# Kernel tuning notes

Measured on AMD Instinct MI355X. Metric: run time of the kernel, lower is better.

Reference implementation:

```python
import jax, jax.numpy as jnp
import numpy as np

NPOINT, RADIUS, NSAMPLE = 512, 0.2, 32
EPS = 1e-5
CHANNELS = [67, 64, 64, 128]


def _fps(pts, npoint):
    # pts: [B, N, 3]; deterministic start at index 0 (torch impl uses randint)
    B, N, _ = pts.shape
    def body(carry, _):
        mind, far = carry
        c = jnp.take_along_axis(pts, far[:, None, None], axis=1)         # [B,1,3]
        mind = jnp.minimum(mind, jnp.sum((pts - c) ** 2, axis=-1))
        return (mind, jnp.argmax(mind, axis=-1).astype(jnp.int32)), far
    init = (jnp.full((B, N), 1e10, pts.dtype), jnp.zeros((B,), jnp.int32))
    _, idxs = jax.lax.scan(body, init, None, length=npoint)
    return idxs.T                                                         # [B, npoint]


def _gather(p, idx):
    # p: [B, N, C], idx: [B, ...] -> [B, ..., C]
    return jax.vmap(lambda pp, ii: pp[ii])(p, idx)


def _cbr(x, w, b, g, be, m, v):
    # Conv3d kernel [1, 4, 1]; torch padding='same' on even kernel -> (lo=1, hi=2) on t axis
    y = jax.lax.conv_general_dilated(x, w, (1, 1, 1),
                                     [(0, 0), (1, 2), (0, 0)],
                                     dimension_numbers=('NCDHW', 'OIDHW', 'NCDHW'))
    ex = lambda a: a[None, :, None, None, None]
    y = y + ex(b)
    # BatchNorm3d (eval mode with running stats)
    y = (y - ex(m)) * ex(g / jnp.sqrt(v + EPS)) + ex(be)
    return jax.nn.relu(y)


def _forward(xyz, points, params):
    B, t, _, N = xyz.shape
    S, K = NPOINT, NSAMPLE
    xf = jnp.transpose(xyz, (0, 1, 3, 2)).reshape(B * t, N, 3)            # [BT,N,3]
    pf = jnp.transpose(points, (0, 1, 3, 2)).reshape(B * t, N, -1)        # [BT,N,D]
    fidx = _fps(xf.reshape(B, t, N, 3)[:, 0], S)                          # [B,S], FPS on frame 0
    fidx_bt = jnp.broadcast_to(fidx[:, None, :], (B, t, S)).reshape(B * t, S)
    new_xyz = _gather(xf, fidx_bt)                                        # [BT,S,3]
    # squared distances via matmul form (matches square_distance)
    sq = (jnp.sum(new_xyz ** 2, -1)[:, :, None] + jnp.sum(xf ** 2, -1)[:, None, :]
          - 2.0 * jnp.einsum('bsc,bnc->bsn', new_xyz, xf))                # [BT,S,N]
    # ball query: invalid -> N, sort indices, take first K, fallback to first valid
    gidx = jnp.where(sq > RADIUS ** 2, N, jnp.arange(N, dtype=jnp.int32)[None, None, :])
    gidx = jnp.sort(gidx, axis=-1)[:, :, :K]                              # [BT,S,K]
    gidx = jnp.where(gidx == N, gidx[:, :, :1], gidx)
    gxyz = _gather(xf, gidx) - new_xyz[:, :, None, :]                     # [BT,S,K,3]
    feat = jnp.concatenate([gxyz, _gather(pf, gidx)], axis=-1)            # [BT,S,K,3+D]
    feat = feat.reshape(B, t, S, K, -1).transpose(0, 4, 2, 1, 3)          # [B,C,S,t,K]
    for p in params:
        feat = _cbr(feat, *p)
    feat = jnp.max(feat, axis=-1)                                         # [B,C',S,t]
    new_points = jnp.transpose(feat, (0, 3, 1, 2))                        # [B,t,C',S]
    new_xyz = new_xyz.reshape(B, t, S, 3).transpose(0, 1, 3, 2)           # [B,t,3,S]
    return new_xyz, new_points


def setup_inputs() -> dict:
    key = jax.random.key(0)
    ks = jax.random.split(key, 40)
    B, t, D, N = 2, 8, 64, 1024
    inp = {
        'xyz': jax.random.uniform(ks[0], (B, t, 3, N), jnp.float32),
        'points': jax.random.normal(ks[1], (B, t, D, N), jnp.float32),
    }
    j = 2
    for i in range(3):
        ci, co = CHANNELS[i], CHANNELS[i + 1]
        inp[f'w{i}'] = jax.random.normal(ks[j], (co, ci, 1, 4, 1), jnp.float32) * 0.05; j += 1
        inp[f'b{i}'] = jax.random.normal(ks[j], (co,), jnp.float32) * 0.01; j += 1
        inp[f'g{i}'] = jax.random.uniform(ks[j], (co,), jnp.float32, 0.5, 1.5); j += 1
        inp[f'be{i}'] = jax.random.normal(ks[j], (co,), jnp.float32) * 0.1; j += 1
        inp[f'm{i}'] = jax.random.normal(ks[j], (co,), jnp.float32) * 0.1; j += 1
        inp[f'v{i}'] = jax.random.uniform(ks[j], (co,), jnp.float32, 0.5, 1.5); j += 1
    return inp


def reference(xyz, points, w0, b0, g0, be0, m0, v0, w1, b1, g1, be1, m1, v1, w2, b2, g2, be2, m2, v2):
    params = [(w0, b0, g0, be0, m0, v0), (w1, b1, g1, be1, m1, v1), (w2, b2, g2, be2, m2, v2)]
    return _forward(xyz, points, params)
```

## Files before the change

### kernel.cpp

```cpp
#include <hip/hip_runtime.h>
#include <math.h>

#define NPTS 1024
#define S_   512
#define T_   8
#define K_   32
#define B_   2

typedef short bf16x8 __attribute__((ext_vector_type(8)));
typedef short short4v __attribute__((ext_vector_type(4)));
typedef float f32x4 __attribute__((ext_vector_type(4)));
typedef float vf2 __attribute__((ext_vector_type(2)));

static __device__ __forceinline__ short f2bf(float f) {
    unsigned u = __float_as_uint(f);
    unsigned r = (u + 0x7FFFu + ((u >> 16) & 1u)) >> 16;
    return (short)r;
}

template <int CTRL>
static __device__ __forceinline__ float dppmaxf(float x) {
    int mv = __builtin_amdgcn_update_dpp(0, __float_as_int(x), CTRL, 0xF, 0xF, true);
    return fmaxf(x, __int_as_float(mv));
}
static __device__ __forceinline__ unsigned wavemax_bits_f(float x) {
    x = dppmaxf<0x111>(x); x = dppmaxf<0x112>(x);
    x = dppmaxf<0x114>(x); x = dppmaxf<0x118>(x);
    x = dppmaxf<0x142>(x); x = dppmaxf<0x143>(x);
    return (unsigned)__builtin_amdgcn_readlane(__float_as_int(x), 63);
}

static __device__ __forceinline__ vf2 pk_sub(vf2 a, vf2 b) { return a - b; }
static __device__ __forceinline__ vf2 pk_fma(vf2 a, vf2 b, vf2 c) {
#if __has_builtin(__builtin_elementwise_fma)
    return __builtin_elementwise_fma(a, b, c);
#else
    vf2 r; r[0] = __fmaf_rn(a[0], b[0], c[0]); r[1] = __fmaf_rn(a[1], b[1], c[1]); return r;
#endif
}
static __device__ __forceinline__ vf2 pk_min(vf2 a, vf2 b) {
#if __has_builtin(__builtin_elementwise_min)
    return __builtin_elementwise_min(a, b);
#else
    vf2 r; r[0] = fminf(a[0], b[0]); r[1] = fminf(a[1], b[1]); return r;
#endif
}
static __device__ __forceinline__ vf2 pk_max(vf2 a, vf2 b) {
#if __has_builtin(__builtin_elementwise_max)
    return __builtin_elementwise_max(a, b);
#else
    vf2 r; r[0] = fmaxf(a[0], b[0]); r[1] = fmaxf(a[1], b[1]); return r;
#endif
}

__global__ __launch_bounds__(64) void fps_kernel(const float* __restrict__ xyz,
                                                 int* __restrict__ fidx)
{
    int b    = blockIdx.x;
    int lane = threadIdx.x;
    __shared__ float4 sc[NPTS];
    const float* bx = xyz + (size_t)b * (T_ * 3 * NPTS);
    vf2 px2[8], py2[8], pz2[8], mind2[8];
#pragma unroll
    for (int q = 0; q < 4; ++q) {
        float4 vx = ((const float4*)(bx))[lane * 4 + q];
        float4 vy = ((const float4*)(bx + NPTS))[lane * 4 + q];
        float4 vz = ((const float4*)(bx + 2 * NPTS))[lane * 4 + q];
        px2[q*2]   = (vf2){vx.x, vx.y};  px2[q*2+1] = (vf2){vx.z, vx.w};
        py2[q*2]   = (vf2){vy.x, vy.y};  py2[q*2+1] = (vf2){vy.z, vy.w};
        pz2[q*2]   = (vf2){vz.x, vz.y};  pz2[q*2+1] = (vf2){vz.z, vz.w};
        int n0 = lane * 16 + q * 4;
        sc[n0+0] = make_float4(vx.x, vy.x, vz.x, 0.f);
        sc[n0+1] = make_float4(vx.y, vy.y, vz.y, 0.f);
        sc[n0+2] = make_float4(vx.z, vy.z, vz.z, 0.f);
        sc[n0+3] = make_float4(vx.w, vy.w, vz.w, 0.f);
        mind2[q*2] = (vf2){1e10f, 1e10f}; mind2[q*2+1] = (vf2){1e10f, 1e10f};
    }
    __syncthreads();

    int far = 0;
    for (int it = 0; it < S_; ++it) {
        if (lane == 0) fidx[b * S_ + it] = far;
        float4 c = sc[far];
        vf2 c2x = (vf2){c.x, c.x}, c2y = (vf2){c.y, c.y}, c2z = (vf2){c.z, c.z};
#pragma unroll
        for (int q = 0; q < 8; ++q) {
            vf2 dx = pk_sub(px2[q], c2x);
            vf2 dy = pk_sub(py2[q], c2y);
            vf2 dz = pk_sub(pz2[q], c2z);
            vf2 d  = pk_fma(dz, dz, pk_fma(dy, dy, dx * dx));
            mind2[q] = pk_min(mind2[q], d);
        }
        vf2 t4a = pk_max(mind2[0], mind2[4]);
        vf2 t4b = pk_max(mind2[1], mind2[5]);
        vf2 t4c = pk_max(mind2[2], mind2[6]);
        vf2 t4d = pk_max(mind2[3], mind2[7]);
        vf2 t2a = pk_max(t4a, t4c);
        vf2 t2b = pk_max(t4b, t4d);
        vf2 t1  = pk_max(t2a, t2b);
        float lmax = fmaxf(t1[0], t1[1]);
        unsigned maxb = wavemax_bits_f(lmax);
        int cj[16];
#pragma unroll
        for (int j = 0; j < 16; ++j)
            cj[j] = (__float_as_uint(mind2[j >> 1][j & 1]) == maxb) ? j : 64;
        int m8[8], m4[4], m2v[2];
#pragma unroll
        for (int j = 0; j < 8; ++j) m8[j] = min(cj[j], cj[j + 8]);
#pragma unroll
        for (int j = 0; j < 4; ++j) m4[j] = min(m8[j], m8[j + 4]);
        m2v[0] = min(m4[0], m4[2]); m2v[1] = min(m4[1], m4[3]);
        int minj = min(m2v[0], m2v[1]);
        unsigned long long mk = __ballot(minj < 64);
        int l0 = __ffsll((long long)mk) - 1;
        int jw = __builtin_amdgcn_readlane(minj, l0);
        far = l0 * 16 + jw;
    }
}

__global__ __launch_bounds__(256) void transpose_points(
    const float* __restrict__ pts, short* __restrict__ ptsT)
{
    int nt = blockIdx.x;
    int bt = blockIdx.y;
    __shared__ float tile[64][65];
    int tid = threadIdx.x;
    for (int e = tid; e < 4096; e += 256) {
        int ci = e >> 6, nn = e & 63;
        tile[ci][nn] = pts[((size_t)bt * 64 + ci) * NPTS + nt * 64 + nn];
    }
    __syncthreads();
    for (int e = tid; e < 4096; e += 256) {
        int nn = e >> 6, ci = e & 63;
        ptsT[((size_t)bt * NPTS + nt * 64 + nn) * 64 + ci] = f2bf(tile[ci][nn]);
    }
}

template <int CI, int CIp, int CO, bool PERM>
__global__ __launch_bounds__(256) void prep_w(const float* __restrict__ w,
                                              short* __restrict__ wg)
{
    int e = blockIdx.x * 256 + threadIdx.x;
    if (e >= 4 * CO * CIp) return;
    int dt = e / (CO * CIp);
    int rem = e - dt * (CO * CIp);
    int co = rem / CIp;
    int ci = rem - co * CIp;
    float val = 0.0f;
    if (PERM) {
        int cref = (ci < 64) ? (ci + 3) : ((ci < 67) ? (ci - 64) : -1);
        if (cref >= 0) val = w[((size_t)co * CI + cref) * 4 + dt];
    } else {
        if (ci < CI) val = w[((size_t)co * CI + ci) * 4 + dt];
    }
    wg[e] = f2bf(val);
}

__global__ __launch_bounds__(256) void conv1_fused(
    const float* __restrict__ xyz, const short* __restrict__ ptsT,
    const int* __restrict__ fidx,
    const short* __restrict__ wg, const float* __restrict__ bb,
    const float* __restrict__ gg, const float* __restrict__ be,
    const float* __restrict__ mm, const float* __restrict__ vv,
    short* __restrict__ actOut, float* __restrict__ out0)
{
    const int CIp = 104, NK = 3, CO = 64;
    __shared__ __align__(16) short xs[256 * 104];
    __shared__ int   gidx_l[8][K_];
    __shared__ float nxyz_l[8][3];
    int s = blockIdx.x, b = blockIdx.y;
    int tid = threadIdx.x;
    int lane = tid & 63;
    int wv   = tid >> 6;

    int fid = fidx[b * S_ + s];
    for (int half = 0; half < 2; ++half) {
        int tt = wv * 2 + half;
        int bt = b * T_ + tt;
        const float* bx = xyz + (size_t)bt * 3 * NPTS;
        float nx = bx[fid], ny = bx[NPTS + fid], nz = bx[2 * NPTS + fid];
        if (lane < 3) {
            float vvv = (lane == 0) ? nx : ((lane == 1) ? ny : nz);
            out0[(bt * 3 + lane) * S_ + s] = vvv;
            nxyz_l[tt][lane] = vvv;
        }
        float A = __fmaf_rn(nz, nz, __fmaf_rn(ny, ny, __fmul_rn(nx, nx)));
        const float R2 = (float)(0.2 * 0.2);
        int count = 0, firstIdx = -1;
        for (int j = 0; j < 16; ++j) {
            if (count >= K_) break;
            int n = j * 64 + lane;
            float x = bx[n], y = bx[NPTS + n], z = bx[2 * NPTS + n];
            float Bn = __fmaf_rn(z, z, __fmaf_rn(y, y, __fmul_rn(x, x)));
            float C  = __fmaf_rn(nz, z, __fmaf_rn(ny, y, __fmul_rn(nx, x)));
            float sq = __fsub_rn(__fadd_rn(A, Bn), __fmul_rn(2.0f, C));
            bool valid = !(sq > R2);
            unsigned long long mb = __ballot(valid);
            if (valid) {
                int pos = count + __popcll(mb & ((1ull << lane) - 1ull));
                if (pos < K_) gidx_l[tt][pos] = n;
            }
            if (firstIdx < 0 && mb) firstIdx = j * 64 + (__ffsll((long long)mb) - 1);
            count += __popcll(mb);
        }
        if (count < K_) {
            for (int p = count + lane; p < K_; p += 64) gidx_l[tt][p] = firstIdx;
        }
    }
    __syncthreads();

    {
        int col = tid;
        int k = col & 31, tt = col >> 5;
        int bt = b * T_ + tt;
        short* xrow = &xs[col * CIp];
        int idx = gidx_l[tt][k];
        const short* prow = ptsT + ((size_t)bt * NPTS + idx) * 64;
#pragma unroll
        for (int c = 0; c < 8; ++c)
            ((int4*)xrow)[c] = ((const int4*)prow)[c];
#pragma unroll
        for (int ci = 0; ci < 3; ++ci)
            xrow[64 + ci] = f2bf(xyz[(size_t)(bt * 3 + ci) * NPTS + idx] - nxyz_l[tt][ci]);
        for (int ci = 67; ci < CIp; ++ci) xrow[ci] = 0;
    }
    __syncthreads();

    int l16 = lane & 15, lq = lane >> 4;
    f32x4 acc[16];
#pragma unroll
    for (int nb = 0; nb < 16; ++nb) acc[nb] = (f32x4){0.f, 0.f, 0.f, 0.f};
#pragma unroll
    for (int ks = 0; ks < NK; ++ks) {
        bf16x8 afr[4];
#pragma unroll
        for (int dt = 0; dt < 4; ++dt)
            afr[dt] = *(const bf16x8*)&wg[((size_t)(dt * CO + wv * 16 + l16)) * CIp + ks * 32 + lq * 8];
        bf16x8 bfr[16];
#pragma unroll
        for (int cb = 0; cb < 16; ++cb)
            bfr[cb] = *(const bf16x8*)&xs[(cb * 16 + l16) * CIp + ks * 32 + lq * 8];
#pragma unroll
        for (int dt = 0; dt < 4; ++dt) {
#pragma unroll
            for (int nb = 0; nb < 16; ++nb) {
                int cb = nb + (dt - 1) * 2;
                if (cb >= 0 && cb < 16)
                    acc[nb] = __builtin_amdgcn_mfma_f32_16x16x32_bf16(
                        afr[dt], bfr[cb], acc[nb], 0, 0, 0);
            }
        }
    }
    float sc[4], c2[4];
#pragma unroll
    for (int j = 0; j < 4; ++j) {
        int co = wv * 16 + lq * 4 + j;
        float scv = gg[co] / sqrtf(vv[co] + 1e-5f);
        sc[j] = scv;
        c2[j] = (bb[co] - mm[co]) * scv + be[co];
    }
#pragma unroll
    for (int nb = 0; nb < 16; ++nb) {
        int col = nb * 16 + l16;
        short4v pk;
#pragma unroll
        for (int j = 0; j < 4; ++j)
            pk[j] = f2bf(fmaxf(acc[nb][j] * sc[j] + c2[j], 0.0f));
        *(short4v*)&actOut[(((size_t)b * S_ + s) * 256 + col) * 64 + wv * 16 + lq * 4] = pk;
    }
}

__global__ __launch_bounds__(256) void conv23_fused(
    const short* __restrict__ actIn,
    const short* __restrict__ wg1, const float* __restrict__ bb1,
    const float* __restrict__ gg1, const float* __restrict__ be1,
    const float* __restrict__ mm1, const float* __restrict__ vv1,
    const short* __restrict__ wg2, const float* __restrict__ bb2,
    const float* __restrict__ gg2, const float* __restrict__ be2,
    const float* __restrict__ mm2, const float* __restrict__ vv2,
    float* __restrict__ outPool)
{
    const int CIp = 72, NK = 2;
    __shared__ __align__(16) short xs2[256 * 72];
    __shared__ __align__(16) short xs3[256 * 72];
    int s = blockIdx.x, b = blockIdx.y;
    int tid = threadIdx.x;
    int lane = tid & 63;
    int wv   = tid >> 6;
    int l16  = lane & 15;
    int lq   = lane >> 4;

    {
        int col = tid;
        short* xrow = &xs2[col * CIp];
        const short* src = actIn + (((size_t)b * S_ + s) * 256 + col) * 64;
#pragma unroll
        for (int c = 0; c < 8; ++c)
            ((int4*)xrow)[c] = ((const int4*)src)[c];
        short* xrow3 = &xs3[col * CIp];
        for (int ci = 64; ci < CIp; ++ci) { xrow[ci] = 0; xrow3[ci] = 0; }
    }
    __syncthreads();

    {
        f32x4 acc[16];
#pragma unroll
        for (int nb = 0; nb < 16; ++nb) acc[nb] = (f32x4){0.f, 0.f, 0.f, 0.f};
#pragma unroll
        for (int ks = 0; ks < NK; ++ks) {
            bf16x8 afr[4];
#pragma unroll
            for (int dt = 0; dt < 4; ++dt)
                afr[dt] = *(const bf16x8*)&wg1[((size_t)(dt * 64 + wv * 16 + l16)) * CIp + ks * 32 + lq * 8];
            bf16x8 bfr[16];
#pragma unroll
            for (int cb = 0; cb < 16; ++cb)
                bfr[cb] = *(const bf16x8*)&xs2[(cb * 16 + l16) * CIp + ks * 32 + lq * 8];
#pragma unroll
            for (int dt = 0; dt < 4; ++dt) {
#pragma unroll
                for (int nb = 0; nb < 16; ++nb) {
                    int cb = nb + (dt - 1) * 2;
                    if (cb >= 0 && cb < 16)
                        acc[nb] = __builtin_amdgcn_mfma_f32_16x16x32_bf16(
                            afr[dt], bfr[cb], acc[nb], 0, 0, 0);
                }
            }
        }
        float sc[4], c2[4];
#pragma unroll
        for (int j = 0; j < 4; ++j) {
            int co = wv * 16 + lq * 4 + j;
            float scv = gg1[co] / sqrtf(vv1[co] + 1e-5f);
            sc[j] = scv;
            c2[j] = (bb1[co] - mm1[co]) * scv + be1[co];
        }
#pragma unroll
        for (int nb = 0; nb < 16; ++nb) {
            int col = nb * 16 + l16;
            short4v pk;
#pragma unroll
            for (int j = 0; j < 4; ++j)
                pk[j] = f2bf(fmaxf(acc[nb][j] * sc[j] + c2[j], 0.0f));
            *(short4v*)&xs3[col * CIp + wv * 16 + lq * 4] = pk;
        }
    }
    __syncthreads();

#pragma unroll
    for (int st = 0; st < 2; ++st) {
        f32x4 acc[16];
#pragma unroll
        for (int nb = 0; nb < 16; ++nb) acc[nb] = (f32x4){0.f, 0.f, 0.f, 0.f};
#pragma unroll
        for (int ks = 0; ks < NK; ++ks) {
            bf16x8 afr[4];
#pragma unroll
            for (int dt = 0; dt < 4; ++dt)
                afr[dt] = *(const bf16x8*)&wg2[((size_t)(dt * 128 + st * 64 + wv * 16 + l16)) * CIp + ks * 32 + lq * 8];
            bf16x8 bfr[16];
#pragma unroll
            for (int cb = 0; cb < 16; ++cb)
                bfr[cb] = *(const bf16x8*)&xs3[(cb * 16 + l16) * CIp + ks * 32 + lq * 8];
#pragma unroll
            for (int dt = 0; dt < 4; ++dt) {
#pragma unroll
                for (int nb = 0; nb < 16; ++nb) {
                    int cb = nb + (dt - 1) * 2;
                    if (cb >= 0 && cb < 16)
                        acc[nb] = __builtin_amdgcn_mfma_f32_16x16x32_bf16(
                            afr[dt], bfr[cb], acc[nb], 0, 0, 0);
                }
            }
        }
        float sc[4], c2[4];
#pragma unroll
        for (int j = 0; j < 4; ++j) {
            int co = st * 64 + wv * 16 + lq * 4 + j;
            float scv = gg2[co] / sqrtf(vv2[co] + 1e-5f);
            sc[j] = scv;
            c2[j] = (bb2[co] - mm2[co]) * scv + be2[co];
        }
#pragma unroll
        for (int nbp = 0; nbp < 8; ++nbp) {
#pragma unroll
            for (int j = 0; j < 4; ++j) {
                float v0 = fmaxf(acc[2 * nbp][j] * sc[j] + c2[j], 0.0f);
                float v1 = fmaxf(acc[2 * nbp + 1][j] * sc[j] + c2[j], 0.0f);
                float v = fmaxf(v0, v1);
#pragma unroll
                for (int off = 1; off < 16; off <<= 1)
                    v = fmaxf(v, __shfl_xor(v, off));
                if (l16 == 0) {
                    int co = st * 64 + wv * 16 + lq * 4 + j;
                    outPool[((size_t)(b * T_ + nbp) * 128 + co) * S_ + s] = v;
                }
            }
        }
    }
}

extern "C" void kernel_launch(void* const* d_in, const int* in_sizes, int n_in,
                              void* d_out, int out_size, void* d_ws, size_t ws_size,
                              hipStream_t stream)
{
    (void)in_sizes; (void)n_in; (void)out_size; (void)ws_size;
    const float* xyz    = (const float*)d_in[0];
    const float* points = (const float*)d_in[1];
    const float* w0 = (const float*)d_in[2];
    const float* b0 = (const float*)d_in[3];
    const float* g0 = (const float*)d_in[4];
    const float* be0 = (const float*)d_in[5];
    const float* m0 = (const float*)d_in[6];
    const float* v0 = (const float*)d_in[7];
    const float* w1 = (const float*)d_in[8];
    const float* b1 = (const float*)d_in[9];
    const float* g1 = (const float*)d_in[10];
    const float* be1 = (const float*)d_in[11];
    const float* m1 = (const float*)d_in[12];
    const float* v1 = (const float*)d_in[13];
    const float* w2 = (const float*)d_in[14];
    const float* b2 = (const float*)d_in[15];
    const float* g2 = (const float*)d_in[16];
    const float* be2 = (const float*)d_in[17];
    const float* m2 = (const float*)d_in[18];
    const float* v2 = (const float*)d_in[19];

    float* out = (float*)d_out;
    char* ws = (char*)d_ws;
    int*   fidx = (int*)ws;
    short* wg0  = (short*)(ws + (size_t)(3 * 1024 * 1024));
    short* wg1  = (short*)(ws + (size_t)(3 * 1024 * 1024) + 256 * 1024);
    short* wg2  = (short*)(ws + (size_t)(3 * 1024 * 1024) + 512 * 1024);
    short* ptsT = (short*)(ws + (size_t)(4  * 1024 * 1024));
    short* actA = (short*)(ws + (size_t)(8  * 1024 * 1024));

    prep_w<67, 104, 64,  true ><<<(4 * 64  * 104 + 255) / 256, 256, 0, stream>>>(w0, wg0);
    prep_w<64, 72,  64,  false><<<(4 * 64  * 72  + 255) / 256, 256, 0, stream>>>(w1, wg1);
    prep_w<64, 72,  128, false><<<(4 * 128 * 72  + 255) / 256, 256, 0, stream>>>(w2, wg2);
    transpose_points<<<dim3(16, B_ * T_), 256, 0, stream>>>(points, ptsT);
    fps_kernel<<<B_, 64, 0, stream>>>(xyz, fidx);

    conv1_fused<<<dim3(S_, B_), 256, 0, stream>>>(
        xyz, ptsT, fidx, wg0, b0, g0, be0, m0, v0, actA, out);
    conv23_fused<<<dim3(S_, B_), 256, 0, stream>>>(
        actA, wg1, b1, g1, be1, m1, v1, wg2, b2, g2, be2, m2, v2,
        out + (size_t)B_ * T_ * 3 * S_);
}
```

Measured before the change: 354.3 us.

## Fuse all three conv stages into one kernel and merge weight prep launches

Measured after the change: 355.0 us. No clear change (+0.2%).

```diff
diff --git a/kernel.cpp b/kernel.cpp
--- a/kernel.cpp
+++ b/kernel.cpp
@@ -136,42 +136,70 @@
     }
 }
 
-template <int CI, int CIp, int CO, bool PERM>
-__global__ __launch_bounds__(256) void prep_w(const float* __restrict__ w,
-                                              short* __restrict__ wg)
+__global__ __launch_bounds__(256) void prep_all(
+    const float* __restrict__ w0, const float* __restrict__ w1,
+    const float* __restrict__ w2,
+    short* __restrict__ wg0, short* __restrict__ wg1, short* __restrict__ wg2)
 {
+    int z = blockIdx.y;
     int e = blockIdx.x * 256 + threadIdx.x;
-    if (e >= 4 * CO * CIp) return;
-    int dt = e / (CO * CIp);
-    int rem = e - dt * (CO * CIp);
-    int co = rem / CIp;
-    int ci = rem - co * CIp;
-    float val = 0.0f;
-    if (PERM) {
+    if (z == 0) {
+        const int CI = 67, CIp = 100, CO = 64;
+        if (e >= 4 * CO * CIp) return;
+        int dt = e / (CO * CIp);
+        int rem = e - dt * (CO * CIp);
+        int co = rem / CIp;
+        int ci = rem - co * CIp;
+        float val = 0.0f;
         int cref = (ci < 64) ? (ci + 3) : ((ci < 67) ? (ci - 64) : -1);
-        if (cref >= 0) val = w[((size_t)co * CI + cref) * 4 + dt];
+        if (cref >= 0) val = w0[((size_t)co * CI + cref) * 4 + dt];
+        wg0[e] = f2bf(val);
+    } else if (z == 1) {
+        const int CI = 64, CIp = 72, CO = 64;
+        if (e >= 4 * CO * CIp) return;
+        int dt = e / (CO * CIp);
+        int rem = e - dt * (CO * CIp);
+        int co = rem / CIp;
+        int ci = rem - co * CIp;
+        wg1[e] = f2bf((ci < CI) ? w1[((size_t)co * CI + ci) * 4 + dt] : 0.0f);
     } else {
-        if (ci < CI) val = w[((size_t)co * CI + ci) * 4 + dt];
-    }
-    wg[e] = f2bf(val);
-}
-
-__global__ __launch_bounds__(256) void conv1_fused(
+        const int CI = 64, CIp = 72, CO = 128;
+        if (e >= 4 * CO * CIp) return;
+        int dt = e / (CO * CIp);
+        int rem = e - dt * (CO * CIp);
+        int co = rem / CIp;
+        int ci = rem - co * CIp;
+        wg2[e] = f2bf((ci < CI) ? w2[((size_t)co * CI + ci) * 4 + dt] : 0.0f);
+    }
+}
+
+__global__ __launch_bounds__(256) void conv123(
     const float* __restrict__ xyz, const short* __restrict__ ptsT,
     const int* __restrict__ fidx,
-    const short* __restrict__ wg, const float* __restrict__ bb,
-    const float* __restrict__ gg, const float* __restrict__ be,
-    const float* __restrict__ mm, const float* __restrict__ vv,
-    short* __restrict__ actOut, float* __restrict__ out0)
+    const short* __restrict__ wg0, const float* __restrict__ bb0,
+    const float* __restrict__ gg0, const float* __restrict__ be0,
+    const float* __restrict__ mm0, const float* __restrict__ vv0,
+    const short* __restrict__ wg1, const float* __restrict__ bb1,
+    const float* __restrict__ gg1, const float* __restrict__ be1,
+    const float* __restrict__ mm1, const float* __restrict__ vv1,
+    const short* __restrict__ wg2, const float* __restrict__ bb2,
+    const float* __restrict__ gg2, const float* __restrict__ be2,
+    const float* __restrict__ mm2, const float* __restrict__ vv2,
+    float* __restrict__ out0, float* __restrict__ outPool)
 {
-    const int CIp = 104, NK = 3, CO = 64;
-    __shared__ __align__(16) short xs[256 * 104];
+    const int CIp1 = 100, NK1 = 3;
+    const int CIp2 = 72,  NK2 = 2;
+    __shared__ __align__(16) short xsA[256 * CIp1];
     __shared__ int   gidx_l[8][K_];
     __shared__ float nxyz_l[8][3];
+    short* xsB = xsA;
+
     int s = blockIdx.x, b = blockIdx.y;
     int tid = threadIdx.x;
     int lane = tid & 63;
     int wv   = tid >> 6;
+    int l16  = lane & 15;
+    int lq   = lane >> 4;
 
     int fid = fidx[b * S_ + s];
     for (int half = 0; half < 2; ++half) {
@@ -187,8 +215,8 @@
         float A = __fmaf_rn(nz, nz, __fmaf_rn(ny, ny, __fmul_rn(nx, nx)));
         const float R2 = (float)(0.2 * 0.2);
         int count = 0, firstIdx = -1;
+#pragma unroll
         for (int j = 0; j < 16; ++j) {
-            if (count >= K_) break;
             int n = j * 64 + lane;
             float x = bx[n], y = bx[NPTS + n], z = bx[2 * NPTS + n];
             float Bn = __fmaf_rn(z, z, __fmaf_rn(y, y, __fmul_rn(x, x)));
@@ -213,7 +241,7 @@
         int col = tid;
         int k = col & 31, tt = col >> 5;
         int bt = b * T_ + tt;
-        short* xrow = &xs[col * CIp];
+        short* xrow = &xsA[col * CIp1];
         int idx = gidx_l[tt][k];
         const short* prow = ptsT + ((size_t)bt * NPTS + idx) * 64;
 #pragma unroll
@@ -222,83 +250,7 @@
 #pragma unroll
         for (int ci = 0; ci < 3; ++ci)
             xrow[64 + ci] = f2bf(xyz[(size_t)(bt * 3 + ci) * NPTS + idx] - nxyz_l[tt][ci]);
-        for (int ci = 67; ci < CIp; ++ci) xrow[ci] = 0;
-    }
-    __syncthreads();
-
-    int l16 = lane & 15, lq = lane >> 4;
-    f32x4 acc[16];
-#pragma unroll
-    for (int nb = 0; nb < 16; ++nb) acc[nb] = (f32x4){0.f, 0.f, 0.f, 0.f};
-#pragma unroll
-    for (int ks = 0; ks < NK; ++ks) {
-        bf16x8 afr[4];
-#pragma unroll
-        for (int dt = 0; dt < 4; ++dt)
-            afr[dt] = *(const bf16x8*)&wg[((size_t)(dt * CO + wv * 16 + l16)) * CIp + ks * 32 + lq * 8];
-        bf16x8 bfr[16];
-#pragma unroll
-        for (int cb = 0; cb < 16; ++cb)
-            bfr[cb] = *(const bf16x8*)&xs[(cb * 16 + l16) * CIp + ks * 32 + lq * 8];
-#pragma unroll
-        for (int dt = 0; dt < 4; ++dt) {
-#pragma unroll
-            for (int nb = 0; nb < 16; ++nb) {
-                int cb = nb + (dt - 1) * 2;
-                if (cb >= 0 && cb < 16)
-                    acc[nb] = __builtin_amdgcn_mfma_f32_16x16x32_bf16(
-                        afr[dt], bfr[cb], acc[nb], 0, 0, 0);
-            }
-        }
-    }
-    float sc[4], c2[4];
-#pragma unroll
-    for (int j = 0; j < 4; ++j) {
-        int co = wv * 16 + lq * 4 + j;
-        float scv = gg[co] / sqrtf(vv[co] + 1e-5f);
-        sc[j] = scv;
-        c2[j] = (bb[co] - mm[co]) * scv + be[co];
-    }
-#pragma unroll
-    for (int nb = 0; nb < 16; ++nb) {
-        int col = nb * 16 + l16;
-        short4v pk;
-#pragma unroll
-        for (int j = 0; j < 4; ++j)
-            pk[j] = f2bf(fmaxf(acc[nb][j] * sc[j] + c2[j], 0.0f));
-        *(short4v*)&actOut[(((size_t)b * S_ + s) * 256 + col) * 64 + wv * 16 + lq * 4] = pk;
-    }
-}
-
-__global__ __launch_bounds__(256) void conv23_fused(
-    const short* __restrict__ actIn,
-    const short* __restrict__ wg1, const float* __restrict__ bb1,
-    const float* __restrict__ gg1, const float* __restrict__ be1,
-    const float* __restrict__ mm1, const float* __restrict__ vv1,
-    const short* __restrict__ wg2, const float* __restrict__ bb2,
-    const float* __restrict__ gg2, const float* __restrict__ be2,
-    const float* __restrict__ mm2, const float* __restrict__ vv2,
-    float* __restrict__ outPool)
-{
-    const int CIp = 72, NK = 2;
-    __shared__ __align__(16) short xs2[256 * 72];
-    __shared__ __align__(16) short xs3[256 * 72];
-    int s = blockIdx.x, b = blockIdx.y;
-    int tid = threadIdx.x;
-    int lane = tid & 63;
-    int wv   = tid >> 6;
-    int l16  = lane & 15;
-    int lq   = lane >> 4;
-
-    {
-        int col = tid;
-        short* xrow = &xs2[col * CIp];
-        const short* src = actIn + (((size_t)b * S_ + s) * 256 + col) * 64;
-#pragma unroll
-        for (int c = 0; c < 8; ++c)
-            ((int4*)xrow)[c] = ((const int4*)src)[c];
-        short* xrow3 = &xs3[col * CIp];
-        for (int ci = 64; ci < CIp; ++ci) { xrow[ci] = 0; xrow3[ci] = 0; }
+        for (int ci = 67; ci < CIp1; ++ci) xrow[ci] = 0;
     }
     __syncthreads();
 
@@ -307,15 +259,15 @@
 #pragma unroll
         for (int nb = 0; nb < 16; ++nb) acc[nb] = (f32x4){0.f, 0.f, 0.f, 0.f};
 #pragma unroll
-        for (int ks = 0; ks < NK; ++ks) {
+        for (int ks = 0; ks < NK1; ++ks) {
             bf16x8 afr[4];
 #pragma unroll
             for (int dt = 0; dt < 4; ++dt)
-                afr[dt] = *(const bf16x8*)&wg1[((size_t)(dt * 64 + wv * 16 + l16)) * CIp + ks * 32 + lq * 8];
+                afr[dt] = *(const bf16x8*)&wg0[((size_t)(dt * 64 + wv * 16 + l16)) * CIp1 + ks * 32 + lq * 8];
             bf16x8 bfr[16];
 #pragma unroll
             for (int cb = 0; cb < 16; ++cb)
-                bfr[cb] = *(const bf16x8*)&xs2[(cb * 16 + l16) * CIp + ks * 32 + lq * 8];
+                bfr[cb] = *(const bf16x8*)&xsA[(cb * 16 + l16) * CIp1 + ks * 32 + lq * 8];
 #pragma unroll
             for (int dt = 0; dt < 4; ++dt) {
 #pragma unroll
@@ -327,6 +279,54 @@
                 }
             }
         }
+        __syncthreads();
+        float sc[4], c2[4];
+#pragma unroll
+        for (int j = 0; j < 4; ++j) {
+            int co = wv * 16 + lq * 4 + j;
+            float scv = gg0[co] / sqrtf(vv0[co] + 1e-5f);
+            sc[j] = scv;
+            c2[j] = (bb0[co] - mm0[co]) * scv + be0[co];
+        }
+#pragma unroll
+        for (int nb = 0; nb < 16; ++nb) {
+            int col = nb * 16 + l16;
+            short4v pk;
+#pragma unroll
+            for (int j = 0; j < 4; ++j)
+                pk[j] = f2bf(fmaxf(acc[nb][j] * sc[j] + c2[j], 0.0f));
+            *(short4v*)&xsB[col * CIp2 + wv * 16 + lq * 4] = pk;
+        }
+        *(int4*)&xsB[tid * CIp2 + 64] = make_int4(0, 0, 0, 0);
+    }
+    __syncthreads();
+
+    {
+        f32x4 acc[16];
+#pragma unroll
+        for (int nb = 0; nb < 16; ++nb) acc[nb] = (f32x4){0.f, 0.f, 0.f, 0.f};
+#pragma unroll
+        for (int ks = 0; ks < NK2; ++ks) {
+            bf16x8 afr[4];
+#pragma unroll
+            for (int dt = 0; dt < 4; ++dt)
+                afr[dt] = *(const bf16x8*)&wg1[((size_t)(dt * 64 + wv * 16 + l16)) * CIp2 + ks * 32 + lq * 8];
+            bf16x8 bfr[16];
+#pragma unroll
+            for (int cb = 0; cb < 16; ++cb)
+                bfr[cb] = *(const bf16x8*)&xsB[(cb * 16 + l16) * CIp2 + ks * 32 + lq * 8];
+#pragma unroll
+            for (int dt = 0; dt < 4; ++dt) {
+#pragma unroll
+                for (int nb = 0; nb < 16; ++nb) {
+                    int cb = nb + (dt - 1) * 2;
+                    if (cb >= 0 && cb < 16)
+                        acc[nb] = __builtin_amdgcn_mfma_f32_16x16x32_bf16(
+                            afr[dt], bfr[cb], acc[nb], 0, 0, 0);
+                }
+            }
+        }
+        __syncthreads();
         float sc[4], c2[4];
 #pragma unroll
         for (int j = 0; j < 4; ++j) {
@@ -342,7 +342,7 @@
 #pragma unroll
             for (int j = 0; j < 4; ++j)
                 pk[j] = f2bf(fmaxf(acc[nb][j] * sc[j] + c2[j], 0.0f));
-            *(short4v*)&xs3[col * CIp + wv * 16 + lq * 4] = pk;
+            *(short4v*)&xsB[col * CIp2 + wv * 16 + lq * 4] = pk;
         }
     }
     __syncthreads();
@@ -353,15 +353,15 @@
 #pragma unroll
         for (int nb = 0; nb < 16; ++nb) acc[nb] = (f32x4){0.f, 0.f, 0.f, 0.f};
 #pragma unroll
-        for (int ks = 0; ks < NK; ++ks) {
+        for (int ks = 0; ks < NK2; ++ks) {
             bf16x8 afr[4];
 #pragma unroll
             for (int dt = 0; dt < 4; ++dt)
-                afr[dt] = *(const bf16x8*)&wg2[((size_t)(dt * 128 + st * 64 + wv * 16 + l16)) * CIp + ks * 32 + lq * 8];
+                afr[dt] = *(const bf16x8*)&wg2[((size_t)(dt * 128 + st * 64 + wv * 16 + l16)) * CIp2 + ks * 32 + lq * 8];
             bf16x8 bfr[16];
 #pragma unroll
             for (int cb = 0; cb < 16; ++cb)
-                bfr[cb] = *(const bf16x8*)&xs3[(cb * 16 + l16) * CIp + ks * 32 + lq * 8];
+                bfr[cb] = *(const bf16x8*)&xsB[(cb * 16 + l16) * CIp2 + ks * 32 + lq * 8];
 #pragma unroll
             for (int dt = 0; dt < 4; ++dt) {
 #pragma unroll
@@ -433,17 +433,15 @@
     short* wg1  = (short*)(ws + (size_t)(3 * 1024 * 1024) + 256 * 1024);
     short* wg2  = (short*)(ws + (size_t)(3 * 1024 * 1024) + 512 * 1024);
     short* ptsT = (short*)(ws + (size_t)(4  * 1024 * 1024));
-    short* actA = (short*)(ws + (size_t)(8  * 1024 * 1024));
-
-    prep_w<67, 104, 64,  true ><<<(4 * 64  * 104 + 255) / 256, 256, 0, stream>>>(w0, wg0);
-    prep_w<64, 72,  64,  false><<<(4 * 64  * 72  + 255) / 256, 256, 0, stream>>>(w1, wg1);
-    prep_w<64, 72,  128, false><<<(4 * 128 * 72  + 255) / 256, 256, 0, stream>>>(w2, wg2);
+
+    prep_all<<<dim3(144, 3), 256, 0, stream>>>(w0, w1, w2, wg0, wg1, wg2);
     transpose_points<<<dim3(16, B_ * T_), 256, 0, stream>>>(points, ptsT);
     fps_kernel<<<B_, 64, 0, stream>>>(xyz, fidx);
 
-    conv1_fused<<<dim3(S_, B_), 256, 0, stream>>>(
-        xyz, ptsT, fidx, wg0, b0, g0, be0, m0, v0, actA, out);
-    conv23_fused<<<dim3(S_, B_), 256, 0, stream>>>(
-        actA, wg1, b1, g1, be1, m1, v1, wg2, b2, g2, be2, m2, v2,
-        out + (size_t)B_ * T_ * 3 * S_);
-}
+    conv123<<<dim3(S_, B_), 256, 0, stream>>>(
+        xyz, ptsT, fidx,
+        wg0, b0, g0, be0, m0, v0,
+        wg1, b1, g1, be1, m1, v1,
+        wg2, b2, g2, be2, m2, v2,
+        out, out + (size_t)B_ * T_ * 3 * S_);
+}
```
